# Kernel tuning notes

Measured on AMD Instinct MI355X. Metric: run time of the kernel, lower is better.

The kernel has to match this reference:

```python
import math
import jax, jax.numpy as jnp
import numpy as np

N = 4096   # num_of_nodes
F = 128    # num_of_features
H = 4      # num_of_heads (GAT layer)
FO = F // 2          # per-head out features = 64
D2 = FO * H          # GATW in features = 256 (heads=1 -> per_head = 256)
V = 16               # num_of_variables
H1 = int(math.sqrt(N)) + 2 * V   # 96
H2 = 2 * V                        # 32


def setup_inputs() -> dict:
    key = jax.random.key(0)
    ks = jax.random.split(key, 20)
    s = 0.05
    inp = {
        "x": jax.random.normal(ks[0], (N, F), jnp.float32),
        "edge_distances": jax.random.uniform(ks[1], (N, N), jnp.float32),
        "spatial_weights": jax.random.uniform(ks[2], (N, N), jnp.float32) - 0.7,
        # GAT layer params
        "Wp1": jax.random.normal(ks[3], (F, H * FO), jnp.float32) * s,
        "a_src1": jax.random.normal(ks[4], (H, FO), jnp.float32) * s,
        "a_tgt1": jax.random.normal(ks[5], (H, FO), jnp.float32) * s,
        "Wskip1": jax.random.normal(ks[6], (F, H * FO), jnp.float32) * s,
        "bias1": jnp.zeros((H * FO,), jnp.float32),
        # GATW layer params (heads=1, per_head=D2)
        "Wp2": jax.random.normal(ks[7], (D2, D2), jnp.float32) * s,
        "a_src2": jax.random.normal(ks[8], (D2,), jnp.float32) * s,
        "a_tgt2": jax.random.normal(ks[9], (D2,), jnp.float32) * s,
        "W1": jax.random.normal(ks[10], (N, H1), jnp.float32) * s,
        "b1": jnp.zeros((H1,), jnp.float32),
        "W2": jax.random.normal(ks[11], (H1, H2), jnp.float32) * s,
        "b2": jnp.zeros((H2,), jnp.float32),
        "W3": jax.random.normal(ks[12], (H2, V), jnp.float32) * s,
        "b3": jnp.zeros((V,), jnp.float32),
        "ols_weights": jax.random.normal(ks[13], (V,), jnp.float32),
        "vertex_x": jax.random.normal(ks[14], (N, V), jnp.float32),
    }
    return inp


def reference(x, edge_distances, spatial_weights,
              Wp1, a_src1, a_tgt1, Wskip1, bias1,
              Wp2, a_src2, a_tgt2,
              W1, b1, W2, b2, W3, b3, ols_weights, vertex_x):
    neg_inf = jnp.float32(-jnp.inf)
    mask = jnp.where(spatial_weights > 0, jnp.float32(0.0), neg_inf)  # (N,N)

    # ---- GATLayer (dropout = identity in eval mode) ----
    p = (x @ Wp1).reshape(N, H, FO)                      # (N,H,FO)
    s_src = jnp.einsum('nhf,hf->hn', p, a_src1)          # (H,N)
    s_tgt = jnp.einsum('nhf,hf->hn', p, a_tgt1)          # (H,N)
    scores = jax.nn.leaky_relu(s_src[:, :, None] + s_tgt[:, None, :], 0.2)  # (H,N,N)
    attn = jax.nn.softmax(scores + mask[None], axis=-1)  # (H,N,N)
    out = jnp.einsum('hij,jhf->ihf', attn, p)            # (N,H,FO)
    out = out + (x @ Wskip1).reshape(N, H, FO)           # skip (dims differ -> proj)
    out = out.reshape(N, H * FO) + bias1
    out = jax.nn.elu(out)                                # (N, D2)

    # ---- GATWLayer (heads=1) ----
    p2 = out @ Wp2                                       # (N, D2)
    ss = p2 @ a_src2                                     # (N,)
    st = p2 @ a_tgt2                                     # (N,)
    nas = jax.nn.relu(ss[:, None] + st[None, :])         # (N,N)
    msw = nas * spatial_weights                          # (N,N), torch shape (1,N,N)

    w = msw                                              # permute(1,2,0).squeeze(-1)
    beta = ((w @ W1 + b1) @ W2 + b2) @ W3 + b3           # (N,V)
    beta = jax.nn.leaky_relu(beta, 0.2)
    beta = beta * ols_weights                            # ols repeated over N
    y_hat = jnp.sum(beta * vertex_x, axis=-1)            # (N,)
    return (beta, y_hat, msw[None])
```

## Files before the change

### kernel.cpp

```cpp
#include <hip/hip_runtime.h>


#define NN 4096
#define FF 128
#define DD2 256
#define NH1 96

typedef __attribute__((ext_vector_type(8))) short bf16x8;
typedef __attribute__((ext_vector_type(4))) float f32x4;

__device__ __forceinline__ short f2bf(float f) {
  unsigned u = __float_as_uint(f);
  u = u + 0x7FFFu + ((u >> 16) & 1u);
  return (short)(u >> 16);
}

#define LOG2E 1.44269504088896340736f

__global__ __launch_bounds__(256) void k1_proj(
    const float* __restrict__ x, const float* __restrict__ Wp1,
    const float* __restrict__ Wsk, const float* __restrict__ bias1,
    const float* __restrict__ as1, const float* __restrict__ at1,
    short* __restrict__ pTf, float* __restrict__ skipb,
    float* __restrict__ s_src, float* __restrict__ s_tgt)
{
  __shared__ float xs[16][FF];
  const int t = threadIdx.x;
  const int r0 = blockIdx.x * 16;
  for (int i = t; i < 16 * FF; i += 256)
    xs[i >> 7][i & 127] = x[(size_t)r0 * FF + i];
  __syncthreads();

  const int c = t;
  float accp[16], accs[16];
#pragma unroll
  for (int i = 0; i < 16; ++i) { accp[i] = 0.f; accs[i] = 0.f; }

  for (int k = 0; k < FF; k += 4) {
    float wp[4], wk[4];
#pragma unroll
    for (int u = 0; u < 4; ++u) {
      wp[u] = Wp1[(size_t)(k + u) * DD2 + c];
      wk[u] = Wsk[(size_t)(k + u) * DD2 + c];
    }
#pragma unroll
    for (int rr = 0; rr < 16; ++rr) {
      const float4 xv = *(const float4*)&xs[rr][k];
      accp[rr] += xv.x * wp[0] + xv.y * wp[1] + xv.z * wp[2] + xv.w * wp[3];
      accs[rr] += xv.x * wk[0] + xv.y * wk[1] + xv.z * wk[2] + xv.w * wk[3];
    }
  }

  const float asv = as1[t], atv = at1[t];
  const float bv = bias1[c];
  const int h = t >> 6;
  const int lane = t & 63;

#pragma unroll
  for (int rr = 0; rr < 16; ++rr)
    skipb[(size_t)(r0 + rr) * DD2 + c] = accs[rr] + bv;

  {
    const int sub = (c >> 4) & 3;
    const int mm = c & 15;
    const int jt32 = r0 >> 5;
    const int qb = (r0 >> 3) & 3;
    short* base = pTf + (size_t)(h * 128 + jt32) * 2048 + (size_t)mm * 8;
#pragma unroll
    for (int g = 0; g < 2; ++g) {
      bf16x8 v;
#pragma unroll
      for (int e = 0; e < 8; ++e) v[e] = f2bf(accp[g * 8 + e]);
      *(bf16x8*)(base + (size_t)(sub * 4 + qb + g) * 128) = v;
    }
  }

#pragma unroll
  for (int rr = 0; rr < 16; ++rr) {
    float ps = accp[rr] * asv, pt = accp[rr] * atv;
#pragma unroll
    for (int off = 32; off > 0; off >>= 1) {
      ps += __shfl_down(ps, off);
      pt += __shfl_down(pt, off);
    }
    if (lane == 0) {
      s_src[h * NN + r0 + rr] = ps * LOG2E;
      s_tgt[h * NN + r0 + rr] = pt * LOG2E;
    }
  }
}

__global__ __launch_bounds__(256) void k2_mask(
    const float* __restrict__ sw, unsigned* __restrict__ maskT)
{
  const int g = blockIdx.x * 256 + threadIdx.x;
  const int i = g >> 7, jw = g & 127;
  const float* p = sw + (size_t)g * 32;
  unsigned bits = 0;
#pragma unroll
  for (int u = 0; u < 8; ++u) {
    const float4 v = *(const float4*)(p + u * 4);
    const unsigned nib = (v.x > 0.f ? 1u : 0u) | (v.y > 0.f ? 2u : 0u)
                       | (v.z > 0.f ? 4u : 0u) | (v.w > 0.f ? 8u : 0u);
    bits |= nib << (u * 4);
  }
  maskT[(size_t)jw * NN + i] = bits;
}

#define K3_STEP(T0, T1, MW, B0, B1, B2, B3) do {                               \
    const float tjv[8] = {T0.x, T0.y, T0.z, T0.w, T1.x, T1.y, T1.z, T1.w};     \
    const unsigned mb = (MW) >> (q * 8);                                       \
    float ev[8]; float esum = 0.f;                                             \
    _Pragma("unroll")                                                          \
    for (int u = 0; u < 8; ++u) {                                              \
      float s = ssrc + tjv[u];                                                 \
      s = fmaxf(s, 0.2f * s);                             \
      const float e = ((mb >> u) & 1u) ? __builtin_amdgcn_exp2f(s) : 0.f;      \
      esum += e; ev[u] = e;                                                    \
    }                                                                          \
    lsum += esum;                                                              \
    union { unsigned u4[4]; bf16x8 v; } af_;                                   \
    _Pragma("unroll")                                                          \
    for (int pp = 0; pp < 4; ++pp)                                             \
      asm("v_cvt_pk_bf16_f32 %0, %1, %2"                                       \
          : "=v"(af_.u4[pp]) : "v"(ev[2 * pp]), "v"(ev[2 * pp + 1]));          \
    acc0 = __builtin_amdgcn_mfma_f32_16x16x32_bf16(af_.v, B0, acc0, 0, 0, 0);  \
    acc1 = __builtin_amdgcn_mfma_f32_16x16x32_bf16(af_.v, B1, acc1, 0, 0, 0);  \
    acc2 = __builtin_amdgcn_mfma_f32_16x16x32_bf16(af_.v, B2, acc2, 0, 0, 0);  \
    acc3 = __builtin_amdgcn_mfma_f32_16x16x32_bf16(af_.v, B3, acc3, 0, 0, 0);  \
  } while (0)

__global__ __launch_bounds__(1024) void k3_attn(
    const short* __restrict__ pTf, const float* __restrict__ s_src,
    const float* __restrict__ s_tgt, const unsigned* __restrict__ maskT,
    float* __restrict__ io )
{
  __shared__ float part[16][16][65];
  __shared__ float lsum_s[16][16];
  const int t = threadIdx.x;
  const int lane = t & 63;
  const int w = t >> 6;
  const int h = w & 3;
  const int qd = w >> 2;
  const int m = lane & 15;
  const int q = lane >> 4;
  const int i0 = blockIdx.x * 16;

  const float ssrc = s_src[h * NN + i0 + m];
  const float* stg = s_tgt + h * NN;
  const unsigned* mcol = maskT + i0 + m;
  const short* pb = pTf + (size_t)h * 128 * 2048 + (size_t)lane * 8;

  f32x4 acc0 = {0.f, 0.f, 0.f, 0.f};
  f32x4 acc1 = acc0, acc2 = acc0, acc3 = acc0;
  float lsum = 0.f;

  const int jq = qd * 1024;
  {
    const int jb = jq + q * 8;
    const int tile0 = jq >> 5;
    float4 ct0 = *(const float4*)(stg + jb);
    float4 ct1 = *(const float4*)(stg + jb + 4);
    unsigned cmw = mcol[(size_t)tile0 * NN];
    const short* cp = pb + (size_t)tile0 * 2048;
    bf16x8 cb0 = *(const bf16x8*)(cp);
    bf16x8 cb1 = *(const bf16x8*)(cp + 512);
    bf16x8 cb2 = *(const bf16x8*)(cp + 1024);
    bf16x8 cb3 = *(const bf16x8*)(cp + 1536);

    for (int jt = jq; jt < jq + 1024 - 32; jt += 32) {
      const int ntile = (jt + 32) >> 5;
      const int njb = jt + 32 + q * 8;
      const float4 nt0 = *(const float4*)(stg + njb);
      const float4 nt1 = *(const float4*)(stg + njb + 4);
      const unsigned nmw = mcol[(size_t)ntile * NN];
      const short* np = pb + (size_t)ntile * 2048;
      const bf16x8 nb0 = *(const bf16x8*)(np);
      const bf16x8 nb1 = *(const bf16x8*)(np + 512);
      const bf16x8 nb2 = *(const bf16x8*)(np + 1024);
      const bf16x8 nb3 = *(const bf16x8*)(np + 1536);
      K3_STEP(ct0, ct1, cmw, cb0, cb1, cb2, cb3);
      ct0 = nt0; ct1 = nt1; cmw = nmw;
      cb0 = nb0; cb1 = nb1; cb2 = nb2; cb3 = nb3;
    }
    K3_STEP(ct0, ct1, cmw, cb0, cb1, cb2, cb3);
  }

  lsum += __shfl_xor(lsum, 16);
  lsum += __shfl_xor(lsum, 32);
  if (q == 0) lsum_s[w][m] = lsum;

  const f32x4 accs[4] = {acc0, acc1, acc2, acc3};
#pragma unroll
  for (int sub = 0; sub < 4; ++sub)
#pragma unroll
    for (int g = 0; g < 4; ++g)
      part[w][q * 4 + g][sub * 16 + m] = accs[sub][g];
  __syncthreads();

  for (int e = t; e < 16 * 256; e += 1024) {
    const int r = e >> 8;
    const int c = e & 255;
    const int hh = c >> 6, cc = c & 63;
    float o = 0.f, l = 0.f;
#pragma unroll
    for (int qq = 0; qq < 4; ++qq) {
      o += part[qq * 4 + hh][r][cc];
      l += lsum_s[qq * 4 + hh][r];
    }
    float z = o / l + io[(size_t)(i0 + r) * DD2 + c];
    z = (z > 0.f) ? z : (__expf(z) - 1.f);
    io[(size_t)(i0 + r) * DD2 + c] = z;
  }
}

__global__ __launch_bounds__(256) void k0_w1t(
    const float* __restrict__ W1g, short* __restrict__ w1t)
{
  __shared__ short st[64 * 97];
  const int t = threadIdx.x;
  const int j0 = blockIdx.x * 64;
  for (int e = t; e < 64 * NH1; e += 256) {
    const int jj = e / NH1, c = e - jj * NH1;
    st[jj * 97 + c] = f2bf(W1g[(size_t)j0 * NH1 + e]);
  }
  __syncthreads();
  for (int o = t; o < NH1 * 32; o += 256) {
    const int c = o >> 5, jj2 = (o & 31) * 2;
    unsigned lo = (unsigned short)st[jj2 * 97 + c];
    unsigned hi = (unsigned short)st[(jj2 + 1) * 97 + c];
    *(unsigned*)(w1t + (size_t)c * NN + j0 + jj2) = lo | (hi << 16);
  }
}

__global__ __launch_bounds__(256) void k4a_vab(
    const float* __restrict__ Wp2, const float* __restrict__ as2,
    const float* __restrict__ at2, float* __restrict__ va, float* __restrict__ vb)
{
  const int lane = threadIdx.x & 63;
  const int w = threadIdx.x >> 6;
  const int r = blockIdx.x * 4 + w;
  const float4 wv = *(const float4*)(Wp2 + (size_t)r * DD2 + lane * 4);
  const float4 a = *(const float4*)(as2 + lane * 4);
  const float4 b = *(const float4*)(at2 + lane * 4);
  float ps = wv.x * a.x + wv.y * a.y + wv.z * a.z + wv.w * a.w;
  float pt = wv.x * b.x + wv.y * b.y + wv.z * b.z + wv.w * b.w;
#pragma unroll
  for (int off = 32; off > 0; off >>= 1) {
    ps += __shfl_down(ps, off);
    pt += __shfl_down(pt, off);
  }
  if (lane == 0) { va[r] = ps; vb[r] = pt; }
}

__global__ __launch_bounds__(256) void k4b_sst(
    const float* __restrict__ oe, const float* __restrict__ va,
    const float* __restrict__ vb, float* __restrict__ ss, float* __restrict__ st)
{
  const int lane = threadIdx.x & 63;
  const int w = threadIdx.x >> 6;
  const int r = blockIdx.x * 4 + w;
  const float4 ov = *(const float4*)(oe + (size_t)r * DD2 + lane * 4);
  const float4 a = *(const float4*)(va + lane * 4);
  const float4 b = *(const float4*)(vb + lane * 4);
  float ps = ov.x * a.x + ov.y * a.y + ov.z * a.z + ov.w * a.w;
  float pt = ov.x * b.x + ov.y * b.y + ov.z * b.z + ov.w * b.w;
#pragma unroll
  for (int off = 32; off > 0; off >>= 1) {
    ps += __shfl_down(ps, off);
    pt += __shfl_down(pt, off);
  }
  if (lane == 0) { ss[r] = ps; st[r] = pt; }
}

__global__ __launch_bounds__(256) void k5_msw(
    const float* __restrict__ ss, const float* __restrict__ st,
    const float* __restrict__ sw, float* __restrict__ msw)
{
  const size_t gid = (size_t)blockIdx.x * 256 + threadIdx.x;
  const int i = (int)(gid >> 10);
  const int j = (int)(gid & 1023) * 4;
  const float s = ss[i];
  const float4 tv = *(const float4*)(st + j);
  const float4 wv = *(const float4*)(sw + (size_t)i * NN + j);
  float4 r;
  r.x = fmaxf(s + tv.x, 0.f) * wv.x;
  r.y = fmaxf(s + tv.y, 0.f) * wv.y;
  r.z = fmaxf(s + tv.z, 0.f) * wv.z;
  r.w = fmaxf(s + tv.w, 0.f) * wv.w;
  *(float4*)(msw + (size_t)i * NN + j) = r;
}

__global__ __launch_bounds__(256) void k6m_mfma(
    const float* __restrict__ msw, const short* __restrict__ w1t,
    float* __restrict__ tmp1)
{
  __shared__ float red[4][16][NH1];
  const int t = threadIdx.x;
  const int w = t >> 6;
  const int lane = t & 63;
  const int m = lane & 15;
  const int q = lane >> 4;
  const int i0 = (blockIdx.x >> 3) * 16;
  const int ja = (blockIdx.x & 7) * 512 + w * 128;

  const float* arow = msw + (size_t)(i0 + m) * NN;
  const short* bbase = w1t + (size_t)m * NN;

  f32x4 acc[6];
#pragma unroll
  for (int n = 0; n < 6; ++n) acc[n] = {0.f, 0.f, 0.f, 0.f};

  for (int jt = ja; jt < ja + 128; jt += 32) {
    const int j8 = jt + q * 8;
    const float4 a0 = *(const float4*)(arow + j8);
    const float4 a1 = *(const float4*)(arow + j8 + 4);
    bf16x8 af;
    af[0] = f2bf(a0.x); af[1] = f2bf(a0.y); af[2] = f2bf(a0.z); af[3] = f2bf(a0.w);
    af[4] = f2bf(a1.x); af[5] = f2bf(a1.y); af[6] = f2bf(a1.z); af[7] = f2bf(a1.w);
#pragma unroll
    for (int n = 0; n < 6; ++n) {
      const bf16x8 bf = *(const bf16x8*)(bbase + (size_t)n * 16 * NN + j8);
      acc[n] = __builtin_amdgcn_mfma_f32_16x16x32_bf16(af, bf, acc[n], 0, 0, 0);
    }
  }

#pragma unroll
  for (int n = 0; n < 6; ++n)
#pragma unroll
    for (int g = 0; g < 4; ++g)
      red[w][q * 4 + g][n * 16 + m] = acc[n][g];
  __syncthreads();

  for (int e = t; e < 16 * NH1; e += 256) {
    const int r = e / NH1, c = e - r * NH1;
    const float s = red[0][r][c] + red[1][r][c] + red[2][r][c] + red[3][r][c];
    atomicAdd(&tmp1[(size_t)(i0 + r) * NH1 + c], s);
  }
}

__global__ __launch_bounds__(256) void k7_head(
    const float* __restrict__ tmp1, const float* __restrict__ b1,
    const float* __restrict__ W2, const float* __restrict__ b2,
    const float* __restrict__ W3, const float* __restrict__ b3,
    const float* __restrict__ ols, const float* __restrict__ vx,
    float* __restrict__ beta, float* __restrict__ yhat)
{
  __shared__ float w2s[96][32];
  __shared__ float w3s[32][16];
  __shared__ float t1s[8][96];
  __shared__ float t2s[8][33];
  const int t = threadIdx.x;
  const int r0 = blockIdx.x * 8;
  for (int i = t; i < 96 * 32; i += 256) w2s[i >> 5][i & 31] = W2[i];
  for (int i = t; i < 32 * 16; i += 256) w3s[i >> 4][i & 15] = W3[i];
  for (int i = t; i < 8 * 96; i += 256) {
    const int rr = i / 96, k = i - rr * 96;
    t1s[rr][k] = tmp1[(size_t)(r0 + rr) * 96 + k] + b1[k];
  }
  __syncthreads();
  {
    const int rr = t >> 5, c2 = t & 31;
    float a = b2[c2];
    for (int k = 0; k < 96; ++k) a += t1s[rr][k] * w2s[k][c2];
    t2s[rr][c2] = a;
  }
  __syncthreads();
  const int rr = t >> 5;
  const int v = t & 31;
  if (v < 16) {
    float z = b3[v];
#pragma unroll
    for (int k = 0; k < 32; ++k) z += t2s[rr][k] * w3s[k][v];
    z = fmaxf(z, 0.2f * z);
    const float bvv = z * ols[v];
    const int r = r0 + rr;
    beta[(size_t)r * 16 + v] = bvv;
    float yv = bvv * vx[(size_t)r * 16 + v];
    yv += __shfl_down(yv, 8);
    yv += __shfl_down(yv, 4);
    yv += __shfl_down(yv, 2);
    yv += __shfl_down(yv, 1);
    if (v == 0) yhat[r] = yv;
  }
}

#define OFF_PT    0u
#define OFF_SKIPB 2097152u
#define OFF_SSRC  6291456u
#define OFF_STGT  6356992u
#define OFF_VA    6422528u
#define OFF_VB    6423552u
#define OFF_SS    6424576u
#define OFF_ST    6440960u
#define OFF_TMP1  6457344u
#define OUT_YHAT 65536
#define OUT_MSW  69632

extern "C" void kernel_launch(void* const* d_in, const int* in_sizes, int n_in,
                              void* d_out, int out_size, void* d_ws, size_t ws_size,
                              hipStream_t stream) {
  const float* x    = (const float*)d_in[0];
  const float* sw   = (const float*)d_in[2];
  const float* Wp1  = (const float*)d_in[3];
  const float* as1  = (const float*)d_in[4];
  const float* at1  = (const float*)d_in[5];
  const float* Wsk  = (const float*)d_in[6];
  const float* bias1= (const float*)d_in[7];
  const float* Wp2  = (const float*)d_in[8];
  const float* as2  = (const float*)d_in[9];
  const float* at2  = (const float*)d_in[10];
  const float* W1   = (const float*)d_in[11];
  const float* b1   = (const float*)d_in[12];
  const float* W2   = (const float*)d_in[13];
  const float* b2   = (const float*)d_in[14];
  const float* W3   = (const float*)d_in[15];
  const float* b3   = (const float*)d_in[16];
  const float* ols  = (const float*)d_in[17];
  const float* vx   = (const float*)d_in[18];

  float* out = (float*)d_out;
  char* ws = (char*)d_ws;
  short* pTf   = (short*)(ws + OFF_PT);
  float* skipb = (float*)(ws + OFF_SKIPB);
  short* w1t   = (short*)(ws + OFF_SKIPB);
  float* s_src = (float*)(ws + OFF_SSRC);
  float* s_tgt = (float*)(ws + OFF_STGT);
  float* va    = (float*)(ws + OFF_VA);
  float* vb    = (float*)(ws + OFF_VB);
  float* ssv   = (float*)(ws + OFF_SS);
  float* stv   = (float*)(ws + OFF_ST);
  float* tmp1  = (float*)(ws + OFF_TMP1);
  unsigned* maskT = (unsigned*)(out + OUT_MSW);

  k1_proj<<<256, 256, 0, stream>>>(x, Wp1, Wsk, bias1, as1, at1, pTf, skipb, s_src, s_tgt);
  k2_mask<<<2048, 256, 0, stream>>>(sw, maskT);
  k3_attn<<<256, 1024, 0, stream>>>(pTf, s_src, s_tgt, maskT, skipb);
  k4a_vab<<<64, 256, 0, stream>>>(Wp2, as2, at2, va, vb);
  k4b_sst<<<1024, 256, 0, stream>>>(skipb, va, vb, ssv, stv);
  k0_w1t<<<64, 256, 0, stream>>>(W1, w1t);
  k5_msw<<<16384, 256, 0, stream>>>(ssv, stv, sw, out + OUT_MSW);
  hipMemsetAsync(tmp1, 0, (size_t)NN * NH1 * sizeof(float), stream);
  k6m_mfma<<<2048, 256, 0, stream>>>(out + OUT_MSW, w1t, tmp1);
  k7_head<<<512, 256, 0, stream>>>(tmp1, b1, W2, b2, W3, b3, ols, vx, out, out + OUT_YHAT);
}
```

Baseline: 319.9 us.

## Fuse msw computation into W1 MFMA kernel and pre-tile W1 for fragment loads

The elementwise msw kernel is merged into the MFMA regression GEMM. Each block computes its 16x512 msw tile, writes it out, and stages a bf16 copy in shared memory for the A operand, so msw is no longer re-read from global memory. W1 is re-laid out into MFMA-fragment order, which makes each B load a contiguous 16-byte per-lane read. The tmp1 memset is folded into the mask kernel, removing one launch. The costs are extra shared memory and barriers, and w1tf now shares workspace with pTf, so it relies on k3 having finished with pTf.

```diff
diff --git a/kernel.cpp b/kernel.cpp
--- a/kernel.cpp
+++ b/kernel.cpp
@@ -91,7 +91,8 @@
 }
 
 __global__ __launch_bounds__(256) void k2_mask(
-    const float* __restrict__ sw, unsigned* __restrict__ maskT)
+    const float* __restrict__ sw, unsigned* __restrict__ maskT,
+    float* __restrict__ tmp1)
 {
   const int g = blockIdx.x * 256 + threadIdx.x;
   const int i = g >> 7, jw = g & 127;
@@ -105,6 +106,7 @@
     bits |= nib << (u * 4);
   }
   maskT[(size_t)jw * NN + i] = bits;
+  if (g < NN * NH1) tmp1[g] = 0.f;
 }
 
 #define K3_STEP(T0, T1, MW, B0, B1, B2, B3) do {                               \
@@ -215,21 +217,28 @@
 }
 
 __global__ __launch_bounds__(256) void k0_w1t(
-    const float* __restrict__ W1g, short* __restrict__ w1t)
-{
-  __shared__ short st[64 * 97];
+    const float* __restrict__ W1g, short* __restrict__ w1tf)
+{
+  __shared__ short stw[64 * 97];
   const int t = threadIdx.x;
   const int j0 = blockIdx.x * 64;
   for (int e = t; e < 64 * NH1; e += 256) {
     const int jj = e / NH1, c = e - jj * NH1;
-    st[jj * 97 + c] = f2bf(W1g[(size_t)j0 * NH1 + e]);
-  }
-  __syncthreads();
-  for (int o = t; o < NH1 * 32; o += 256) {
-    const int c = o >> 5, jj2 = (o & 31) * 2;
-    unsigned lo = (unsigned short)st[jj2 * 97 + c];
-    unsigned hi = (unsigned short)st[(jj2 + 1) * 97 + c];
-    *(unsigned*)(w1t + (size_t)c * NN + j0 + jj2) = lo | (hi << 16);
+    stw[jj * 97 + c] = f2bf(W1g[(size_t)(j0 + jj) * NH1 + c]);
+  }
+  __syncthreads();
+  for (int o = t; o < 768; o += 256) {
+    const int m = o & 15;
+    const int rest = o >> 4;
+    const int q = rest & 3;
+    const int tn = rest >> 2;
+    const int tile = tn / 6, n = tn - tile * 6;
+    bf16x8 v;
+#pragma unroll
+    for (int e8 = 0; e8 < 8; ++e8)
+      v[e8] = stw[(tile * 32 + q * 8 + e8) * 97 + n * 16 + m];
+    *(bf16x8*)(w1tf + (size_t)((j0 >> 5) + tile) * 3072 + n * 512
+               + (size_t)(q * 16 + m) * 8) = v;
   }
 }
 
@@ -273,68 +282,74 @@
   if (lane == 0) { ss[r] = ps; st[r] = pt; }
 }
 
-__global__ __launch_bounds__(256) void k5_msw(
-    const float* __restrict__ ss, const float* __restrict__ st,
-    const float* __restrict__ sw, float* __restrict__ msw)
-{
-  const size_t gid = (size_t)blockIdx.x * 256 + threadIdx.x;
-  const int i = (int)(gid >> 10);
-  const int j = (int)(gid & 1023) * 4;
-  const float s = ss[i];
-  const float4 tv = *(const float4*)(st + j);
-  const float4 wv = *(const float4*)(sw + (size_t)i * NN + j);
-  float4 r;
-  r.x = fmaxf(s + tv.x, 0.f) * wv.x;
-  r.y = fmaxf(s + tv.y, 0.f) * wv.y;
-  r.z = fmaxf(s + tv.z, 0.f) * wv.z;
-  r.w = fmaxf(s + tv.w, 0.f) * wv.w;
-  *(float4*)(msw + (size_t)i * NN + j) = r;
-}
-
-__global__ __launch_bounds__(256) void k6m_mfma(
-    const float* __restrict__ msw, const short* __restrict__ w1t,
-    float* __restrict__ tmp1)
-{
-  __shared__ float red[4][16][NH1];
+__global__ __launch_bounds__(256) void k56_fused(
+    const float* __restrict__ ss, const float* __restrict__ stv,
+    const float* __restrict__ sw, const short* __restrict__ w1tf,
+    float* __restrict__ msw, float* __restrict__ tmp1)
+{
+  __shared__ union {
+    ushort a[16][520];
+    float red[4][16][NH1];
+  } sh;
   const int t = threadIdx.x;
   const int w = t >> 6;
   const int lane = t & 63;
   const int m = lane & 15;
   const int q = lane >> 4;
   const int i0 = (blockIdx.x >> 3) * 16;
-  const int ja = (blockIdx.x & 7) * 512 + w * 128;
-
-  const float* arow = msw + (size_t)(i0 + m) * NN;
-  const short* bbase = w1t + (size_t)m * NN;
+  const int j0 = (blockIdx.x & 7) * 512;
+
+#pragma unroll
+  for (int it = 0; it < 8; ++it) {
+    const int idx = it * 256 + t;
+    const int row = idx >> 7;
+    const int colf = idx & 127;
+    const int j = j0 + colf * 4;
+    const float ssv = ss[i0 + row];
+    const float4 wv = *(const float4*)(sw + (size_t)(i0 + row) * NN + j);
+    const float4 tv = *(const float4*)(stv + j);
+    float4 v;
+    v.x = fmaxf(ssv + tv.x, 0.f) * wv.x;
+    v.y = fmaxf(ssv + tv.y, 0.f) * wv.y;
+    v.z = fmaxf(ssv + tv.z, 0.f) * wv.z;
+    v.w = fmaxf(ssv + tv.w, 0.f) * wv.w;
+    *(float4*)(msw + (size_t)(i0 + row) * NN + j) = v;
+    unsigned p0, p1;
+    asm("v_cvt_pk_bf16_f32 %0, %1, %2" : "=v"(p0) : "v"(v.x), "v"(v.y));
+    asm("v_cvt_pk_bf16_f32 %0, %1, %2" : "=v"(p1) : "v"(v.z), "v"(v.w));
+    uint2 pk; pk.x = p0; pk.y = p1;
+    *(uint2*)&sh.a[row][colf * 4] = pk;
+  }
+  __syncthreads();
 
   f32x4 acc[6];
 #pragma unroll
   for (int n = 0; n < 6; ++n) acc[n] = {0.f, 0.f, 0.f, 0.f};
 
-  for (int jt = ja; jt < ja + 128; jt += 32) {
-    const int j8 = jt + q * 8;
-    const float4 a0 = *(const float4*)(arow + j8);
-    const float4 a1 = *(const float4*)(arow + j8 + 4);
-    bf16x8 af;
-    af[0] = f2bf(a0.x); af[1] = f2bf(a0.y); af[2] = f2bf(a0.z); af[3] = f2bf(a0.w);
-    af[4] = f2bf(a1.x); af[5] = f2bf(a1.y); af[6] = f2bf(a1.z); af[7] = f2bf(a1.w);
+#pragma unroll
+  for (int kk = 0; kk < 128; kk += 32) {
+    const int jloc = w * 128 + kk;
+    const bf16x8 af = *(const bf16x8*)&sh.a[m][jloc + q * 8];
+    const short* wt = w1tf + (size_t)((j0 + jloc) >> 5) * 3072 + (size_t)lane * 8;
 #pragma unroll
     for (int n = 0; n < 6; ++n) {
-      const bf16x8 bf = *(const bf16x8*)(bbase + (size_t)n * 16 * NN + j8);
+      const bf16x8 bf = *(const bf16x8*)(wt + n * 512);
       acc[n] = __builtin_amdgcn_mfma_f32_16x16x32_bf16(af, bf, acc[n], 0, 0, 0);
     }
   }
+  __syncthreads();
 
 #pragma unroll
   for (int n = 0; n < 6; ++n)
 #pragma unroll
     for (int g = 0; g < 4; ++g)
-      red[w][q * 4 + g][n * 16 + m] = acc[n][g];
+      sh.red[w][q * 4 + g][n * 16 + m] = acc[n][g];
   __syncthreads();
 
   for (int e = t; e < 16 * NH1; e += 256) {
     const int r = e / NH1, c = e - r * NH1;
-    const float s = red[0][r][c] + red[1][r][c] + red[2][r][c] + red[3][r][c];
+    const float s = sh.red[0][r][c] + sh.red[1][r][c]
+                  + sh.red[2][r][c] + sh.red[3][r][c];
     atomicAdd(&tmp1[(size_t)(i0 + r) * NH1 + c], s);
   }
 }
@@ -422,8 +437,8 @@
   float* out = (float*)d_out;
   char* ws = (char*)d_ws;
   short* pTf   = (short*)(ws + OFF_PT);
+  short* w1tf  = (short*)(ws + OFF_PT);
   float* skipb = (float*)(ws + OFF_SKIPB);
-  short* w1t   = (short*)(ws + OFF_SKIPB);
   float* s_src = (float*)(ws + OFF_SSRC);
   float* s_tgt = (float*)(ws + OFF_STGT);
   float* va    = (float*)(ws + OFF_VA);
@@ -434,13 +449,11 @@
   unsigned* maskT = (unsigned*)(out + OUT_MSW);
 
   k1_proj<<<256, 256, 0, stream>>>(x, Wp1, Wsk, bias1, as1, at1, pTf, skipb, s_src, s_tgt);
-  k2_mask<<<2048, 256, 0, stream>>>(sw, maskT);
+  k2_mask<<<2048, 256, 0, stream>>>(sw, maskT, tmp1);
   k3_attn<<<256, 1024, 0, stream>>>(pTf, s_src, s_tgt, maskT, skipb);
+  k0_w1t<<<64, 256, 0, stream>>>(W1, w1tf);
   k4a_vab<<<64, 256, 0, stream>>>(Wp2, as2, at2, va, vb);
   k4b_sst<<<1024, 256, 0, stream>>>(skipb, va, vb, ssv, stv);
-  k0_w1t<<<64, 256, 0, stream>>>(W1, w1t);
-  k5_msw<<<16384, 256, 0, stream>>>(ssv, stv, sw, out + OUT_MSW);
-  hipMemsetAsync(tmp1, 0, (size_t)NN * NH1 * sizeof(float), stream);
-  k6m_mfma<<<2048, 256, 0, stream>>>(out + OUT_MSW, w1t, tmp1);
+  k56_fused<<<2048, 256, 0, stream>>>(ssv, stv, sw, w1tf, out + OUT_MSW, tmp1);
   k7_head<<<512, 256, 0, stream>>>(tmp1, b1, W2, b2, W3, b3, ols, vx, out, out + OUT_YHAT);
 }
```

New measurement: 293.7 us. 8.2% less time.
